# Performance work log

Hardware: AMD Instinct MI355X
Metric: run time of the kernel (lower is better)

The kernel has to match this reference:

```python
import jax, jax.numpy as jnp
import numpy as np

ALPHA = 0.1
HIDDEN = 512


def setup_inputs() -> dict:
    key = jax.random.key(0)
    k1, k2, k3 = jax.random.split(key, 3)
    input_size = 256
    x = jax.random.normal(k1, (64, 1024, input_size), dtype=jnp.float32)
    W = jax.random.normal(k2, (HIDDEN, HIDDEN), dtype=jnp.float32) / jnp.sqrt(jnp.float32(HIDDEN))
    U = jax.random.normal(k3, (HIDDEN, input_size), dtype=jnp.float32) / jnp.sqrt(jnp.float32(HIDDEN))
    return {"x": x, "W": W, "U": U}


def reference(x, W, U):
    # x: [B, T, I]; recurrence h <- h + alpha * (-h + tanh(h) @ W^T + x_t @ U^T)
    B, T, I = x.shape
    alpha = jnp.float32(ALPHA)
    # precompute input projection for all timesteps: [B, T, H]
    xu = jnp.einsum('bti,hi->bth', x, U)

    def step(h, xu_t):
        dh = -h + jnp.tanh(h) @ W.T + xu_t
        h = h + alpha * dh
        return h, h

    h0 = jnp.zeros((B, W.shape[0]), dtype=x.dtype)
    _, hiddens = jax.lax.scan(step, h0, jnp.swapaxes(xu, 0, 1))  # [T, B, H]
    return jnp.swapaxes(hiddens, 0, 1)  # [B, T, H]
```

## Files before the change

### kernel.cpp

```cpp
#include <hip/hip_runtime.h>

typedef __attribute__((ext_vector_type(4))) float f32x4;
typedef __attribute__((ext_vector_type(8))) short short8;
typedef __attribute__((ext_vector_type(4))) short short4_t;

__device__ __forceinline__ short f2bf(float f) {
  unsigned u = __float_as_uint(f);
  u += 0x7fffu + ((u >> 16) & 1u);
  return (short)(u >> 16);
}

__device__ __forceinline__ float tanh_fast(float x) {
  float e = __expf(2.0f * x);
  return 1.0f - __fdividef(2.0f, e + 1.0f);
}

__global__ __launch_bounds__(256) void convert_wu(
    const float* __restrict__ W, const float* __restrict__ U,
    short* __restrict__ Wb, short* __restrict__ Ub) {
  int i = blockIdx.x * 256 + threadIdx.x;
  if (i < 65536) {
    f32x4 v = ((const f32x4*)W)[i];
    short4_t s;
    s.x = f2bf(v.x); s.y = f2bf(v.y); s.z = f2bf(v.z); s.w = f2bf(v.w);
    ((short4_t*)Wb)[i] = s;
  } else if (i < 98304) {
    int k = i - 65536;
    f32x4 v = ((const f32x4*)U)[k];
    short4_t s;
    s.x = f2bf(v.x); s.y = f2bf(v.y); s.z = f2bf(v.z); s.w = f2bf(v.w);
    ((short4_t*)Ub)[k] = s;
  }
}

__global__ __launch_bounds__(256) void xu_gemm(
    const float* __restrict__ x, const short* __restrict__ Ub,
    float* __restrict__ out) {
  __shared__ __attribute__((aligned(16))) short a_lds[128][272];
  __shared__ __attribute__((aligned(16))) short b_lds[128][272];
  const int tid = threadIdx.x;
  const int mb = blockIdx.x >> 2;
  const int nb = blockIdx.x & 3;

  const float* xb = x + (size_t)mb * (128 * 256);
  for (int c = 0; c < 32; ++c) {
    int idx = c * 256 + tid;
    int r = idx >> 6, c4 = idx & 63;
    f32x4 v = ((const f32x4*)xb)[idx];
    short4_t s;
    s.x = f2bf(v.x); s.y = f2bf(v.y); s.z = f2bf(v.z); s.w = f2bf(v.w);
    *(short4_t*)&a_lds[r][c4 * 4] = s;
  }
  const short* ub = Ub + nb * (128 * 256);
  for (int c = 0; c < 16; ++c) {
    int idx = c * 256 + tid;
    int r = idx >> 5, ch = idx & 31;
    *(short8*)&b_lds[r][ch * 8] = ((const short8*)ub)[idx];
  }
  __syncthreads();

  const int lane = tid & 63, wave = tid >> 6;
  const int wr = wave >> 1, wc = wave & 1;
  const int lr = lane & 15, lk = lane >> 4;
  const f32x4 zero = {0.f, 0.f, 0.f, 0.f};
  f32x4 acc[4][4];
  #pragma unroll
  for (int mt = 0; mt < 4; ++mt)
    #pragma unroll
    for (int nt = 0; nt < 4; ++nt) acc[mt][nt] = zero;

  #pragma unroll
  for (int kt = 0; kt < 8; ++kt) {
    const int k = kt * 32 + lk * 8;
    short8 a[4], b[4];
    #pragma unroll
    for (int mt = 0; mt < 4; ++mt)
      a[mt] = *(const short8*)&a_lds[wr * 64 + mt * 16 + lr][k];
    #pragma unroll
    for (int nt = 0; nt < 4; ++nt)
      b[nt] = *(const short8*)&b_lds[wc * 64 + nt * 16 + lr][k];
    #pragma unroll
    for (int mt = 0; mt < 4; ++mt)
      #pragma unroll
      for (int nt = 0; nt < 4; ++nt)
        acc[mt][nt] = __builtin_amdgcn_mfma_f32_16x16x32_bf16(a[mt], b[nt], acc[mt][nt], 0, 0, 0);
  }

  #pragma unroll
  for (int mt = 0; mt < 4; ++mt)
    #pragma unroll
    for (int nt = 0; nt < 4; ++nt)
      #pragma unroll
      for (int q = 0; q < 4; ++q) {
        int row = mb * 128 + wr * 64 + mt * 16 + lk * 4 + q;
        int col = nb * 128 + wc * 64 + nt * 16 + lr;
        out[(size_t)row * 512 + col] = acc[mt][nt][q];
      }
}

__global__ __launch_bounds__(512)
__attribute__((amdgpu_waves_per_eu(2, 2)))
void rnn_scan(const short* __restrict__ Wb, float* __restrict__ out) {
  __shared__ __attribute__((aligned(16))) short w_lds[512][136];
  __shared__ __attribute__((aligned(16))) short a_lds[16][520];
  const int tid = threadIdx.x;
  const int blk = blockIdx.x;
  const int lane = tid & 63, wave = tid >> 6;
  const int j0 = wave * 64;
  const int lr = lane & 15, lk = lane >> 4;

  short8 wreg[4][12];
  #pragma unroll
  for (int jt = 0; jt < 4; ++jt) {
    const short* wrow = Wb + (j0 + jt * 16 + lr) * 512 + lk * 8;
    #pragma unroll
    for (int kt = 0; kt < 12; ++kt) {
      wreg[jt][kt] = *(const short8*)(wrow + kt * 32);
      asm volatile("" : "+v"(wreg[jt][kt]));
    }
  }

  for (int c = 0; c < 16; ++c) {
    int idx = c * 512 + tid;
    int j = idx >> 4, ch = idx & 15;
    *(short8*)&w_lds[j][ch * 8] = *(const short8*)(Wb + j * 512 + 384 + ch * 8);
  }

  float h[4][4];
  #pragma unroll
  for (int jt = 0; jt < 4; ++jt)
    #pragma unroll
    for (int q = 0; q < 4; ++q) h[jt][q] = 0.f;

  const size_t base = (size_t)(blk * 16 + lk * 4) * 524288 + j0 + lr;
  __syncthreads();

  f32x4 acc[4];
  {
    const float* p = out + base;
    #pragma unroll
    for (int jt = 0; jt < 4; ++jt)
      #pragma unroll
      for (int q = 0; q < 4; ++q)
        acc[jt][q] = p[(size_t)q * 524288 + jt * 16];
  }

  for (int t = 0; t < 1024; ++t) {
    #pragma unroll
    for (int jt = 0; jt < 4; ++jt)
      #pragma unroll
      for (int q = 0; q < 4; ++q)
        a_lds[lk * 4 + q][j0 + jt * 16 + lr] = f2bf(tanh_fast(h[jt][q]));
    __syncthreads();

    #pragma unroll
    for (int kt = 0; kt < 16; ++kt) {
      short8 a8 = *(const short8*)&a_lds[lr][kt * 32 + lk * 8];
      if (kt < 12) {
        #pragma unroll
        for (int jt = 0; jt < 4; ++jt)
          acc[jt] = __builtin_amdgcn_mfma_f32_16x16x32_bf16(a8, wreg[jt][kt], acc[jt], 0, 0, 0);
      } else {
        #pragma unroll
        for (int jt = 0; jt < 4; ++jt) {
          short8 b = *(const short8*)&w_lds[j0 + jt * 16 + lr][(kt - 12) * 32 + lk * 8];
          acc[jt] = __builtin_amdgcn_mfma_f32_16x16x32_bf16(a8, b, acc[jt], 0, 0, 0);
        }
      }
    }

    float* po = out + base + (size_t)t * 512;
    #pragma unroll
    for (int jt = 0; jt < 4; ++jt)
      #pragma unroll
      for (int q = 0; q < 4; ++q) {
        float v = 0.9f * h[jt][q] + 0.1f * acc[jt][q];
        h[jt][q] = v;
        po[(size_t)q * 524288 + jt * 16] = v;
      }
    __syncthreads();

    int tn = t + 1; if (tn > 1023) tn = 1023;
    const float* pn = out + base + (size_t)tn * 512;
    #pragma unroll
    for (int jt = 0; jt < 4; ++jt)
      #pragma unroll
      for (int q = 0; q < 4; ++q)
        acc[jt][q] = pn[(size_t)q * 524288 + jt * 16];
  }
}

extern "C" void kernel_launch(void* const* d_in, const int* in_sizes, int n_in,
                              void* d_out, int out_size, void* d_ws, size_t ws_size,
                              hipStream_t stream) {
  (void)in_sizes; (void)n_in; (void)out_size; (void)ws_size;
  const float* x = (const float*)d_in[0];
  const float* W = (const float*)d_in[1];
  const float* U = (const float*)d_in[2];
  float* out = (float*)d_out;
  short* Wb = (short*)d_ws;
  short* Ub = Wb + 512 * 512;

  convert_wu<<<384, 256, 0, stream>>>(W, U, Wb, Ub);
  xu_gemm<<<2048, 256, 0, stream>>>(x, Ub, out);
  rnn_scan<<<4, 512, 0, stream>>>(Wb, out);
}
```

Baseline: 3.184 ms.

## Stream most of W from global/L2 per step instead of keeping it in registers

Cuts the register-resident slice of W from 12 K-tiles to 2 and keeps 4 K-tiles in LDS. The remaining 10 K-tiles are now streamed from global memory (L2) every timestep with a two-deep software prefetch. This frees many VGPRs and changes launch bounds to allow two blocks per CU. The cost is that every one of the 1024 sequential steps now issues global loads sitting on the critical path of the recurrence.

```diff
diff --git a/kernel.cpp b/kernel.cpp
--- a/kernel.cpp
+++ b/kernel.cpp
@@ -98,9 +98,8 @@
       }
 }
 
-__global__ __launch_bounds__(512)
-__attribute__((amdgpu_waves_per_eu(2, 2)))
-void rnn_scan(const short* __restrict__ Wb, float* __restrict__ out) {
+__global__ __launch_bounds__(512, 2) void rnn_scan(
+    const short* __restrict__ Wb, float* __restrict__ out) {
   __shared__ __attribute__((aligned(16))) short w_lds[512][136];
   __shared__ __attribute__((aligned(16))) short a_lds[16][520];
   const int tid = threadIdx.x;
@@ -109,21 +108,26 @@
   const int j0 = wave * 64;
   const int lr = lane & 15, lk = lane >> 4;
 
-  short8 wreg[4][12];
+  short8 wreg[4][2];
   #pragma unroll
   for (int jt = 0; jt < 4; ++jt) {
     const short* wrow = Wb + (j0 + jt * 16 + lr) * 512 + lk * 8;
     #pragma unroll
-    for (int kt = 0; kt < 12; ++kt) {
+    for (int kt = 0; kt < 2; ++kt) {
       wreg[jt][kt] = *(const short8*)(wrow + kt * 32);
       asm volatile("" : "+v"(wreg[jt][kt]));
     }
   }
+
+  const short* pj[4];
+  #pragma unroll
+  for (int jt = 0; jt < 4; ++jt)
+    pj[jt] = Wb + (j0 + jt * 16 + lr) * 512 + lk * 8;
 
   for (int c = 0; c < 16; ++c) {
     int idx = c * 512 + tid;
     int j = idx >> 4, ch = idx & 15;
-    *(short8*)&w_lds[j][ch * 8] = *(const short8*)(Wb + j * 512 + 384 + ch * 8);
+    *(short8*)&w_lds[j][ch * 8] = *(const short8*)(Wb + j * 512 + 64 + ch * 8);
   }
 
   float h[4][4];
@@ -153,18 +157,48 @@
         a_lds[lk * 4 + q][j0 + jt * 16 + lr] = f2bf(tanh_fast(h[jt][q]));
     __syncthreads();
 
-    #pragma unroll
-    for (int kt = 0; kt < 16; ++kt) {
+    short8 s0[4], s1[4];
+    #pragma unroll
+    for (int jt = 0; jt < 4; ++jt) s0[jt] = *(const short8*)(pj[jt] + 6 * 32);
+    #pragma unroll
+    for (int jt = 0; jt < 4; ++jt) s1[jt] = *(const short8*)(pj[jt] + 7 * 32);
+
+    #pragma unroll
+    for (int kt = 0; kt < 2; ++kt) {
       short8 a8 = *(const short8*)&a_lds[lr][kt * 32 + lk * 8];
-      if (kt < 12) {
+      #pragma unroll
+      for (int jt = 0; jt < 4; ++jt)
+        acc[jt] = __builtin_amdgcn_mfma_f32_16x16x32_bf16(a8, wreg[jt][kt], acc[jt], 0, 0, 0);
+    }
+    #pragma unroll
+    for (int kt = 2; kt < 6; ++kt) {
+      short8 a8 = *(const short8*)&a_lds[lr][kt * 32 + lk * 8];
+      #pragma unroll
+      for (int jt = 0; jt < 4; ++jt) {
+        short8 b = *(const short8*)&w_lds[j0 + jt * 16 + lr][(kt - 2) * 32 + lk * 8];
+        acc[jt] = __builtin_amdgcn_mfma_f32_16x16x32_bf16(a8, b, acc[jt], 0, 0, 0);
+      }
+    }
+    #pragma unroll
+    for (int kt = 6; kt < 16; ++kt) {
+      short8 a8 = *(const short8*)&a_lds[lr][kt * 32 + lk * 8];
+      if ((kt & 1) == 0) {
         #pragma unroll
         for (int jt = 0; jt < 4; ++jt)
-          acc[jt] = __builtin_amdgcn_mfma_f32_16x16x32_bf16(a8, wreg[jt][kt], acc[jt], 0, 0, 0);
+          acc[jt] = __builtin_amdgcn_mfma_f32_16x16x32_bf16(a8, s0[jt], acc[jt], 0, 0, 0);
+        if (kt + 2 < 16) {
+          #pragma unroll
+          for (int jt = 0; jt < 4; ++jt)
+            s0[jt] = *(const short8*)(pj[jt] + (kt + 2) * 32);
+        }
       } else {
         #pragma unroll
-        for (int jt = 0; jt < 4; ++jt) {
-          short8 b = *(const short8*)&w_lds[j0 + jt * 16 + lr][(kt - 12) * 32 + lk * 8];
-          acc[jt] = __builtin_amdgcn_mfma_f32_16x16x32_bf16(a8, b, acc[jt], 0, 0, 0);
+        for (int jt = 0; jt < 4; ++jt)
+          acc[jt] = __builtin_amdgcn_mfma_f32_16x16x32_bf16(a8, s1[jt], acc[jt], 0, 0, 0);
+        if (kt + 2 < 16) {
+          #pragma unroll
+          for (int jt = 0; jt < 4; ++jt)
+            s1[jt] = *(const short8*)(pj[jt] + (kt + 2) * 32);
         }
       }
     }
```

Result: no change. 3.159 ms (-0.8%).

## Halve scan waves and split W across registers, LDS and streamed global loads

Applied to the files above, without the earlier changes.

The recurrent scan now runs 4 waves of 256 threads instead of 8, each wave owning 128 output columns. W is split three ways: K-tiles 0-8 stay in VGPRs, tiles 9-12 sit in LDS, and tiles 13-15 are streamed from global/L2 through a rotating register buffer. The loads for the next tile are issued while the current MFMAs run. This aims to cut per-step barrier cost and wave count on the latency-bound serial loop, but it raises register pressure and puts global loads on the critical path of every timestep.

```diff
diff --git a/kernel.cpp b/kernel.cpp
--- a/kernel.cpp
+++ b/kernel.cpp
@@ -98,80 +98,112 @@
       }
 }
 
-__global__ __launch_bounds__(512)
-__attribute__((amdgpu_waves_per_eu(2, 2)))
+__global__ __launch_bounds__(256, 1)
+__attribute__((amdgpu_waves_per_eu(1, 1)))
 void rnn_scan(const short* __restrict__ Wb, float* __restrict__ out) {
   __shared__ __attribute__((aligned(16))) short w_lds[512][136];
   __shared__ __attribute__((aligned(16))) short a_lds[16][520];
   const int tid = threadIdx.x;
-  const int blk = blockIdx.x;
+  const int g = blockIdx.x;
   const int lane = tid & 63, wave = tid >> 6;
-  const int j0 = wave * 64;
+  const int jb = wave * 128;
   const int lr = lane & 15, lk = lane >> 4;
 
-  short8 wreg[4][12];
-  #pragma unroll
-  for (int jt = 0; jt < 4; ++jt) {
-    const short* wrow = Wb + (j0 + jt * 16 + lr) * 512 + lk * 8;
-    #pragma unroll
-    for (int kt = 0; kt < 12; ++kt) {
-      wreg[jt][kt] = *(const short8*)(wrow + kt * 32);
+  const short* ps[8];
+  #pragma unroll
+  for (int jt = 0; jt < 8; ++jt)
+    ps[jt] = Wb + (jb + jt * 16 + lr) * 512 + lk * 8;
+
+  short8 wreg[8][9];
+  #pragma unroll
+  for (int jt = 0; jt < 8; ++jt)
+    #pragma unroll
+    for (int kt = 0; kt < 9; ++kt) {
+      wreg[jt][kt] = *(const short8*)(ps[jt] + kt * 32);
       asm volatile("" : "+v"(wreg[jt][kt]));
     }
-  }
-
-  for (int c = 0; c < 16; ++c) {
-    int idx = c * 512 + tid;
+
+  for (int c = 0; c < 32; ++c) {
+    int idx = c * 256 + tid;
     int j = idx >> 4, ch = idx & 15;
-    *(short8*)&w_lds[j][ch * 8] = *(const short8*)(Wb + j * 512 + 384 + ch * 8);
-  }
-
-  float h[4][4];
-  #pragma unroll
-  for (int jt = 0; jt < 4; ++jt)
+    *(short8*)&w_lds[j][ch * 8] = *(const short8*)(Wb + j * 512 + 288 + ch * 8);
+  }
+
+  float h[8][4];
+  #pragma unroll
+  for (int jt = 0; jt < 8; ++jt)
     #pragma unroll
     for (int q = 0; q < 4; ++q) h[jt][q] = 0.f;
 
-  const size_t base = (size_t)(blk * 16 + lk * 4) * 524288 + j0 + lr;
+  const size_t base = (size_t)(g * 16 + lk * 4) * 524288 + jb + lr;
   __syncthreads();
 
-  f32x4 acc[4];
+  f32x4 acc[8];
   {
     const float* p = out + base;
     #pragma unroll
-    for (int jt = 0; jt < 4; ++jt)
+    for (int jt = 0; jt < 8; ++jt)
       #pragma unroll
       for (int q = 0; q < 4; ++q)
         acc[jt][q] = p[(size_t)q * 524288 + jt * 16];
   }
 
+  short8 sbuf[8];
+  #pragma unroll
+  for (int jt = 0; jt < 8; ++jt) sbuf[jt] = *(const short8*)(ps[jt] + 13 * 32);
+
   for (int t = 0; t < 1024; ++t) {
     #pragma unroll
-    for (int jt = 0; jt < 4; ++jt)
+    for (int jt = 0; jt < 8; ++jt)
       #pragma unroll
       for (int q = 0; q < 4; ++q)
-        a_lds[lk * 4 + q][j0 + jt * 16 + lr] = f2bf(tanh_fast(h[jt][q]));
+        a_lds[lk * 4 + q][jb + jt * 16 + lr] = f2bf(tanh_fast(h[jt][q]));
     __syncthreads();
 
-    #pragma unroll
-    for (int kt = 0; kt < 16; ++kt) {
+    {
+      short8 a8 = *(const short8*)&a_lds[lr][13 * 32 + lk * 8];
+      #pragma unroll
+      for (int jt = 0; jt < 8; ++jt)
+        acc[jt] = __builtin_amdgcn_mfma_f32_16x16x32_bf16(a8, sbuf[jt], acc[jt], 0, 0, 0);
+      #pragma unroll
+      for (int jt = 0; jt < 8; ++jt) sbuf[jt] = *(const short8*)(ps[jt] + 14 * 32);
+    }
+    #pragma unroll
+    for (int kt = 9; kt < 13; ++kt) {
       short8 a8 = *(const short8*)&a_lds[lr][kt * 32 + lk * 8];
-      if (kt < 12) {
-        #pragma unroll
-        for (int jt = 0; jt < 4; ++jt)
-          acc[jt] = __builtin_amdgcn_mfma_f32_16x16x32_bf16(a8, wreg[jt][kt], acc[jt], 0, 0, 0);
-      } else {
-        #pragma unroll
-        for (int jt = 0; jt < 4; ++jt) {
-          short8 b = *(const short8*)&w_lds[j0 + jt * 16 + lr][(kt - 12) * 32 + lk * 8];
-          acc[jt] = __builtin_amdgcn_mfma_f32_16x16x32_bf16(a8, b, acc[jt], 0, 0, 0);
-        }
+      #pragma unroll
+      for (int jt = 0; jt < 8; ++jt) {
+        short8 b = *(const short8*)&w_lds[jb + jt * 16 + lr][(kt - 9) * 32 + lk * 8];
+        acc[jt] = __builtin_amdgcn_mfma_f32_16x16x32_bf16(a8, b, acc[jt], 0, 0, 0);
       }
     }
+    {
+      short8 a8 = *(const short8*)&a_lds[lr][14 * 32 + lk * 8];
+      #pragma unroll
+      for (int jt = 0; jt < 8; ++jt)
+        acc[jt] = __builtin_amdgcn_mfma_f32_16x16x32_bf16(a8, sbuf[jt], acc[jt], 0, 0, 0);
+      #pragma unroll
+      for (int jt = 0; jt < 8; ++jt) sbuf[jt] = *(const short8*)(ps[jt] + 15 * 32);
+    }
+    #pragma unroll
+    for (int kt = 0; kt < 9; ++kt) {
+      short8 a8 = *(const short8*)&a_lds[lr][kt * 32 + lk * 8];
+      #pragma unroll
+      for (int jt = 0; jt < 8; ++jt)
+        acc[jt] = __builtin_amdgcn_mfma_f32_16x16x32_bf16(a8, wreg[jt][kt], acc[jt], 0, 0, 0);
+    }
+    {
+      short8 a8 = *(const short8*)&a_lds[lr][15 * 32 + lk * 8];
+      #pragma unroll
+      for (int jt = 0; jt < 8; ++jt)
+        acc[jt] = __builtin_amdgcn_mfma_f32_16x16x32_bf16(a8, sbuf[jt], acc[jt], 0, 0, 0);
+      #pragma unroll
+      for (int jt = 0; jt < 8; ++jt) sbuf[jt] = *(const short8*)(ps[jt] + 13 * 32);
+    }
 
     float* po = out + base + (size_t)t * 512;
     #pragma unroll
-    for (int jt = 0; jt < 4; ++jt)
+    for (int jt = 0; jt < 8; ++jt)
       #pragma unroll
       for (int q = 0; q < 4; ++q) {
         float v = 0.9f * h[jt][q] + 0.1f * acc[jt][q];
@@ -183,7 +215,7 @@
     int tn = t + 1; if (tn > 1023) tn = 1023;
     const float* pn = out + base + (size_t)tn * 512;
     #pragma unroll
-    for (int jt = 0; jt < 4; ++jt)
+    for (int jt = 0; jt < 8; ++jt)
       #pragma unroll
       for (int q = 0; q < 4; ++q)
         acc[jt][q] = pn[(size_t)q * 524288 + jt * 16];
@@ -203,5 +235,5 @@
 
   convert_wu<<<384, 256, 0, stream>>>(W, U, Wb, Ub);
   xu_gemm<<<2048, 256, 0, stream>>>(x, Ub, out);
-  rnn_scan<<<4, 512, 0, stream>>>(Wb, out);
-}
+  rnn_scan<<<4, 256, 0, stream>>>(Wb, out);
+}
```

Measured after the change: 4.592 ms. 44.2% more time.
